# Kernel optimization log

Measured on AMD Instinct MI355X. Metric: run time of the kernel, lower is better.

Reference implementation:

```python
import jax, jax.numpy as jnp
import numpy as np

D_MODEL = 1024
NUM_HEADS = 16
HEAD_DIM = D_MODEL // NUM_HEADS
THETA = 10000.0


def setup_inputs() -> dict:
    key = jax.random.key(0)
    k1, k2, k3 = jax.random.split(key, 3)
    B, S = 4, 2048
    x = jax.random.normal(k1, (B, S, D_MODEL), dtype=jnp.float32)
    token_positions = jnp.arange(S, dtype=jnp.int32)
    std_qkv = 2.0 / (D_MODEL + 3 * D_MODEL)
    std_o = 2.0 / (D_MODEL + D_MODEL)
    W_qkv = jax.random.normal(k2, (3 * D_MODEL, D_MODEL), dtype=jnp.float32) * std_qkv
    W_o = jax.random.normal(k3, (D_MODEL, D_MODEL), dtype=jnp.float32) * std_o
    return {"x": x, "token_positions": token_positions, "W_qkv": W_qkv, "W_o": W_o}


def _apply_rope(x, positions):
    # x: [B, H, S, d]; positions: [S]
    d = x.shape[-1]
    inv_freq = 1.0 / THETA ** (2.0 * jnp.arange(0, d // 2, dtype=jnp.float32) / d)
    angle = positions.astype(jnp.float32)[:, None] * inv_freq[None, :]  # [S, d/2]
    cos, sin = jnp.cos(angle), jnp.sin(angle)
    x1, x2 = x[..., 0::2], x[..., 1::2]
    rot = jnp.stack([x1 * cos - x2 * sin, x2 * cos + x1 * sin], axis=-1)
    return rot.reshape(x.shape)


def reference(x, token_positions, W_qkv, W_o):
    B, S, D = x.shape
    H, hd = NUM_HEADS, HEAD_DIM
    qkv = jnp.einsum('bsi,ji->bsj', x, W_qkv)            # [B, S, 3D]
    qkv = qkv.reshape(B, S, 3, H, hd).transpose(2, 0, 3, 1, 4)  # [3, B, H, S, hd]
    q, k, v = qkv[0], qkv[1], qkv[2]
    q = _apply_rope(q, token_positions)
    k = _apply_rope(k, token_positions)
    scores = jnp.einsum('bhqd,bhkd->bhqk', q, k) / jnp.sqrt(jnp.float32(hd))
    causal = jnp.tril(jnp.ones((S, S), dtype=bool))
    scores = jnp.where(causal, scores, -jnp.inf)
    probs = jax.nn.softmax(scores, axis=-1)
    attn = jnp.einsum('bhqk,bhkd->bhqd', probs, v)       # [B, H, S, hd]
    attn = attn.transpose(0, 2, 1, 3).reshape(B, S, D)
    return jnp.einsum('bsi,ji->bsj', attn, W_o)
```

## Files before the change

kernel.cpp:

```cpp
#include <hip/hip_runtime.h>

#define B_ 4
#define S_ 2048
#define D_ 1024
#define H_ 16
#define HD_ 64
#define M_ (B_*S_)
#define NQKV_ (3*D_)

typedef _Float16 f16;
typedef __attribute__((ext_vector_type(4))) _Float16 f16x4;
typedef __attribute__((ext_vector_type(8))) _Float16 f16x8;
typedef __attribute__((ext_vector_type(4))) float f32x4;

__device__ __forceinline__ void gload_lds16(const void* g, void* lds) {
  __builtin_amdgcn_global_load_lds(
      (const __attribute__((address_space(1))) void*)g,
      (__attribute__((address_space(3))) void*)lds, 16, 0, 0);
}

__global__ void cast_kernel(const float* __restrict__ in, f16* __restrict__ out) {
  size_t i = (size_t)(blockIdx.x * 256 + threadIdx.x) * 8;
  float4 a = *reinterpret_cast<const float4*>(in + i);
  float4 b = *reinterpret_cast<const float4*>(in + i + 4);
  f16x8 o;
  o[0] = (f16)a.x; o[1] = (f16)a.y; o[2] = (f16)a.z; o[3] = (f16)a.w;
  o[4] = (f16)b.x; o[5] = (f16)b.y; o[6] = (f16)b.z; o[7] = (f16)b.w;
  *reinterpret_cast<f16x8*>(out + i) = o;
}

__global__ void trig_kernel(const int* __restrict__ pos, float2* __restrict__ tab) {
  int idx = blockIdx.x * 256 + threadIdx.x;
  int s = idx >> 5, t = idx & 31;
  float p = (float)pos[s];
  float invf = exp2f((float)t * -0.4152410118609203f);
  float sn, cs;
  sincosf(p * invf, &sn, &cs);
  tab[idx] = float2{cs, sn};
}

template <int MODE>
__global__ __launch_bounds__(256)
void gemm_bt(const f16* __restrict__ A, const f16* __restrict__ Bt,
             void* __restrict__ Cout, const float2* __restrict__ tab,
             f16* __restrict__ kout, f16* __restrict__ vtout,
             int M, int N, int K) {
  __shared__ __align__(16) f16 As[128 * 64];
  __shared__ __align__(16) f16 Bs[128 * 64];
  const int tid = threadIdx.x;
  const int w = tid >> 6, l = tid & 63;
  const int nM = M >> 7;
  const int bm = (blockIdx.x % nM) << 7;
  const int bn = (blockIdx.x / nM) << 7;
  const int wr = (w >> 1) << 6;
  const int wc = (w & 1) << 6;
  const int lr = l & 15;
  const int lk = (l >> 4) << 3;
  const int orow = (l >> 4) << 2;
  const int srow = tid >> 3;
  const int sc8 = (tid & 7) * 8;

  f32x4 acc[4][4];
  #pragma unroll
  for (int i = 0; i < 4; ++i)
    #pragma unroll
    for (int j = 0; j < 4; ++j) acc[i][j] = f32x4{0.f, 0.f, 0.f, 0.f};

  for (int k0 = 0; k0 < K; k0 += 64) {
    __syncthreads();
    #pragma unroll
    for (int i = 0; i < 4; ++i) {
      gload_lds16(A + (size_t)(bm + i * 32 + srow) * K + k0 + sc8,
                  (void*)(As + (i * 256 + w * 64) * 8));
      gload_lds16(Bt + (size_t)(bn + i * 32 + srow) * K + k0 + sc8,
                  (void*)(Bs + (i * 256 + w * 64) * 8));
    }
    __syncthreads();
    #pragma unroll
    for (int t = 0; t < 2; ++t) {
      f16x8 af[4], bfr[4];
      #pragma unroll
      for (int mi = 0; mi < 4; ++mi)
        af[mi] = *reinterpret_cast<const f16x8*>(As + (wr + mi * 16 + lr) * 64 + t * 32 + lk);
      #pragma unroll
      for (int ni = 0; ni < 4; ++ni)
        bfr[ni] = *reinterpret_cast<const f16x8*>(Bs + (wc + ni * 16 + lr) * 64 + t * 32 + lk);
      #pragma unroll
      for (int mi = 0; mi < 4; ++mi)
        #pragma unroll
        for (int ni = 0; ni < 4; ++ni)
          acc[mi][ni] = __builtin_amdgcn_mfma_f32_16x16x32_f16(bfr[ni], af[mi], acc[mi][ni], 0, 0, 0);
    }
  }

  if (MODE == 0) {
    const int which = bn >> 10;
    const int h = ((bn + wc) >> 6) & (H_ - 1);
    if (which < 2) {
      f16* dst = which ? kout : (f16*)Cout;
      const float qs = which ? 1.0f : 0.125f * 1.4426950408889634f;
      #pragma unroll
      for (int mi = 0; mi < 4; ++mi) {
        int m = bm + wr + mi * 16 + lr;
        int b = m >> 11, s = m & (S_ - 1);
        size_t rowbase = ((size_t)(b * H_ + h) * S_ + s) * HD_;
        const float4* trow = reinterpret_cast<const float4*>(tab + (size_t)s * 32);
        #pragma unroll
        for (int ni = 0; ni < 4; ++ni) {
          int d0 = ni * 16 + orow;
          float4 cssn = trow[d0 >> 2];
          float x0 = acc[mi][ni][0], x1 = acc[mi][ni][1];
          float x2 = acc[mi][ni][2], x3 = acc[mi][ni][3];
          f16x4 ov;
          ov[0] = (f16)((x0 * cssn.x - x1 * cssn.y) * qs);
          ov[1] = (f16)((x1 * cssn.x + x0 * cssn.y) * qs);
          ov[2] = (f16)((x2 * cssn.z - x3 * cssn.w) * qs);
          ov[3] = (f16)((x3 * cssn.z + x2 * cssn.w) * qs);
          *reinterpret_cast<f16x4*>(&dst[rowbase + d0]) = ov;
        }
      }
    } else {
      #pragma unroll
      for (int mi = 0; mi < 4; ++mi) {
        int m = bm + wr + mi * 16 + lr;
        int b = m >> 11, s = m & (S_ - 1);
        size_t base = (size_t)(b * H_ + h) * (HD_ * S_) + s;
        #pragma unroll
        for (int ni = 0; ni < 4; ++ni)
          #pragma unroll
          for (int r = 0; r < 4; ++r)
            vtout[base + (size_t)(ni * 16 + orow + r) * S_] = (f16)acc[mi][ni][r];
      }
    }
  } else {
    float* C = (float*)Cout;
    #pragma unroll
    for (int mi = 0; mi < 4; ++mi) {
      int m = bm + wr + mi * 16 + lr;
      #pragma unroll
      for (int ni = 0; ni < 4; ++ni) {
        int n = bn + wc + ni * 16 + orow;
        *reinterpret_cast<float4*>(&C[(size_t)m * N + n]) =
            float4{acc[mi][ni][0], acc[mi][ni][1], acc[mi][ni][2], acc[mi][ni][3]};
      }
    }
  }
}

__global__ __launch_bounds__(256)
void attn_kernel(const f16* __restrict__ q, const f16* __restrict__ k,
                 const f16* __restrict__ vt, f16* __restrict__ attn_out) {
  __shared__ __align__(16) f16 Ks[64 * 64];
  __shared__ __align__(16) f16 Vs[64 * 64];
  __shared__ __align__(16) f16 Ps[4][16 * 72];
  const int tid = threadIdx.x, w = tid >> 6, l = tid & 63;
  const int lr = l & 15, lk = (l >> 4) << 3, orow = (l >> 4) << 2;
  const int bh = blockIdx.x & 63;
  const int qt = 31 - (int)(blockIdx.x >> 6);
  const int q0 = qt << 6;
  const size_t bhoff = (size_t)bh * (S_ * HD_);
  const size_t vtoff = (size_t)bh * (HD_ * S_);
  const int srow = tid >> 3;
  const int sc8 = (tid & 7) * 8;
  const int ssw = sc8 ^ ((srow & 7) << 3);
  const int swz = (lr & 7) << 3;
  const int h = bh & (H_ - 1), b = bh >> 4;
  const int qg = q0 + w * 16 + lr;

  f16x8 qf[2];
  #pragma unroll
  for (int t = 0; t < 2; ++t)
    qf[t] = *reinterpret_cast<const f16x8*>(q + bhoff + (size_t)qg * HD_ + t * 32 + lk);

  f32x4 o[4];
  float m_run = -1e30f, l_run = 0.f;
  #pragma unroll
  for (int i = 0; i < 4; ++i) o[i] = f32x4{0.f, 0.f, 0.f, 0.f};

  const int ntiles = qt + 1;
  for (int it = 0; it < ntiles; ++it) {
    const int kv0 = it << 6;
    __syncthreads();
    #pragma unroll
    for (int i = 0; i < 2; ++i) {
      gload_lds16(k + bhoff + (size_t)(kv0 + i * 32 + srow) * HD_ + ssw,
                  (void*)(Ks + (i * 256 + w * 64) * 8));
      gload_lds16(vt + vtoff + (size_t)(i * 32 + srow) * S_ + kv0 + ssw,
                  (void*)(Vs + (i * 256 + w * 64) * 8));
    }
    __syncthreads();

    f32x4 sacc[4];
    #pragma unroll
    for (int ni = 0; ni < 4; ++ni) sacc[ni] = f32x4{0.f, 0.f, 0.f, 0.f};
    #pragma unroll
    for (int t = 0; t < 2; ++t) {
      #pragma unroll
      for (int ni = 0; ni < 4; ++ni) {
        f16x8 kf = *reinterpret_cast<const f16x8*>(Ks + (ni * 16 + lr) * 64 + ((t * 32 + lk) ^ swz));
        sacc[ni] = __builtin_amdgcn_mfma_f32_16x16x32_f16(kf, qf[t], sacc[ni], 0, 0, 0);
      }
    }
    if (it == ntiles - 1) {
      #pragma unroll
      for (int ni = 0; ni < 4; ++ni) {
        #pragma unroll
        for (int r = 0; r < 4; ++r) {
          int kvg = kv0 + ni * 16 + orow + r;
          if (kvg > qg) sacc[ni][r] = -1e30f;
        }
      }
    }

    f32x4 m4 = sacc[0];
    #pragma unroll
    for (int ni = 1; ni < 4; ++ni)
      #pragma unroll
      for (int r = 0; r < 4; ++r) m4[r] = fmaxf(m4[r], sacc[ni][r]);
    float mloc = fmaxf(fmaxf(m4[0], m4[1]), fmaxf(m4[2], m4[3]));
    mloc = fmaxf(mloc, __shfl_xor(mloc, 16));
    mloc = fmaxf(mloc, __shfl_xor(mloc, 32));
    float mn = fmaxf(m_run, mloc);
    float scale = exp2f(m_run - mn);
    m_run = mn;
    #pragma unroll
    for (int ni = 0; ni < 4; ++ni)
      #pragma unroll
      for (int r = 0; r < 4; ++r) sacc[ni][r] = exp2f(sacc[ni][r] - mn);
    f32x4 s4 = sacc[0];
    #pragma unroll
    for (int ni = 1; ni < 4; ++ni)
      #pragma unroll
      for (int r = 0; r < 4; ++r) s4[r] += sacc[ni][r];
    float sloc = (s4[0] + s4[1]) + (s4[2] + s4[3]);
    sloc += __shfl_xor(sloc, 16);
    sloc += __shfl_xor(sloc, 32);
    l_run = l_run * scale + sloc;
    #pragma unroll
    for (int ni = 0; ni < 4; ++ni)
      #pragma unroll
      for (int r = 0; r < 4; ++r) o[ni][r] *= scale;

    #pragma unroll
    for (int ni = 0; ni < 4; ++ni) {
      f16x4 pk;
      #pragma unroll
      for (int r = 0; r < 4; ++r) pk[r] = (f16)sacc[ni][r];
      *reinterpret_cast<f16x4*>(&Ps[w][lr * 72 + ni * 16 + orow]) = pk;
    }

    #pragma unroll
    for (int t = 0; t < 2; ++t) {
      f16x8 pf = *reinterpret_cast<const f16x8*>(&Ps[w][lr * 72 + t * 32 + lk]);
      #pragma unroll
      for (int ni = 0; ni < 4; ++ni) {
        f16x8 vf = *reinterpret_cast<const f16x8*>(Vs + (ni * 16 + lr) * 64 + ((t * 32 + lk) ^ swz));
        o[ni] = __builtin_amdgcn_mfma_f32_16x16x32_f16(vf, pf, o[ni], 0, 0, 0);
      }
    }
  }

  float rl = 1.0f / l_run;
  #pragma unroll
  for (int ni = 0; ni < 4; ++ni) {
    f16x4 ov;
    #pragma unroll
    for (int r = 0; r < 4; ++r) ov[r] = (f16)(o[ni][r] * rl);
    *reinterpret_cast<f16x4*>(
        &attn_out[(size_t)(b * S_ + qg) * D_ + h * HD_ + ni * 16 + orow]) = ov;
  }
}

extern "C" void kernel_launch(void* const* d_in, const int* in_sizes, int n_in,
                              void* d_out, int out_size, void* d_ws, size_t ws_size,
                              hipStream_t stream) {
  const float* x    = (const float*)d_in[0];
  const int*   pos  = (const int*)d_in[1];
  const float* wqkv = (const float*)d_in[2];
  const float* wo   = (const float*)d_in[3];
  float* out = (float*)d_out;

  const size_t BHSD = (size_t)B_ * H_ * S_ * HD_;
  f16* xb    = (f16*)d_ws;
  f16* wqkvb = xb + (size_t)M_ * D_;
  f16* wob   = wqkvb + (size_t)NQKV_ * D_;
  f16* qb    = wob + (size_t)D_ * D_;
  f16* kb    = qb + BHSD;
  f16* vtb   = kb + BHSD;
  f16* attnb = vtb + BHSD;
  float2* tab = (float2*)(attnb + BHSD);

  cast_kernel<<<(M_ * D_) / 2048, 256, 0, stream>>>(x, xb);
  cast_kernel<<<(NQKV_ * D_) / 2048, 256, 0, stream>>>(wqkv, wqkvb);
  cast_kernel<<<(D_ * D_) / 2048, 256, 0, stream>>>(wo, wob);
  trig_kernel<<<(S_ * 32) / 256, 256, 0, stream>>>(pos, tab);

  gemm_bt<0><<<(M_ / 128) * (NQKV_ / 128), 256, 0, stream>>>(
      xb, wqkvb, (void*)qb, tab, kb, vtb, M_, NQKV_, D_);

  attn_kernel<<<64 * 32, 256, 0, stream>>>(qb, kb, vtb, attnb);

  gemm_bt<1><<<(M_ / 128) * (D_ / 128), 256, 0, stream>>>(
      attnb, wob, (void*)out, nullptr, nullptr, nullptr, M_, D_, D_);
}
```

Before: 216.2 us.

## Use 32x32x16 MFMA with 128-row query tiles in attention kernel

Switches the flash-attention kernel from 16x16x32 MFMAs with 64-query tiles to 32x32x16 MFMAs with 128-query tiles, so each wave handles 32 query rows. Each K/V tile loaded into LDS is now reused by twice as many queries, halving K/V traffic per query. Waves whose rows lie entirely before the current KV tile skip the compute. The P buffer gets an XOR swizzle, and the launch-bounds hint asks for 4 blocks per CU. The risks are higher register pressure from 16-wide accumulators, half as many blocks to spread over the GPU, and idle waves on the diagonal tiles.

```diff
diff --git a/kernel.cpp b/kernel.cpp
--- a/kernel.cpp
+++ b/kernel.cpp
@@ -12,6 +12,7 @@
 typedef __attribute__((ext_vector_type(4))) _Float16 f16x4;
 typedef __attribute__((ext_vector_type(8))) _Float16 f16x8;
 typedef __attribute__((ext_vector_type(4))) float f32x4;
+typedef __attribute__((ext_vector_type(16))) float f32x16;
 
 __device__ __forceinline__ void gload_lds16(const void* g, void* lds) {
   __builtin_amdgcn_global_load_lds(
@@ -147,128 +148,138 @@
   }
 }
 
-__global__ __launch_bounds__(256)
+__global__ __launch_bounds__(256, 4)
 void attn_kernel(const f16* __restrict__ q, const f16* __restrict__ k,
                  const f16* __restrict__ vt, f16* __restrict__ attn_out) {
   __shared__ __align__(16) f16 Ks[64 * 64];
   __shared__ __align__(16) f16 Vs[64 * 64];
-  __shared__ __align__(16) f16 Ps[4][16 * 72];
-  const int tid = threadIdx.x, w = tid >> 6, l = tid & 63;
-  const int lr = l & 15, lk = (l >> 4) << 3, orow = (l >> 4) << 2;
+  __shared__ __align__(16) f16 Ps[4][32 * 64];
+  const int tid = threadIdx.x, wq = tid >> 6, l = tid & 63;
+  const int lq = l & 31, hi = l >> 5;
   const int bh = blockIdx.x & 63;
-  const int qt = 31 - (int)(blockIdx.x >> 6);
-  const int q0 = qt << 6;
+  const int qt = 15 - (int)(blockIdx.x >> 6);
+  const int q0 = qt << 7;
   const size_t bhoff = (size_t)bh * (S_ * HD_);
   const size_t vtoff = (size_t)bh * (HD_ * S_);
   const int srow = tid >> 3;
   const int sc8 = (tid & 7) * 8;
   const int ssw = sc8 ^ ((srow & 7) << 3);
-  const int swz = (lr & 7) << 3;
+  const int swz = (lq & 7) << 3;
   const int h = bh & (H_ - 1), b = bh >> 4;
-  const int qg = q0 + w * 16 + lr;
-
-  f16x8 qf[2];
+  const int wqmin = q0 + wq * 32;
+  const int qrow = wqmin + lq;
+
+  f16x8 qf[4];
   #pragma unroll
-  for (int t = 0; t < 2; ++t)
-    qf[t] = *reinterpret_cast<const f16x8*>(q + bhoff + (size_t)qg * HD_ + t * 32 + lk);
-
-  f32x4 o[4];
+  for (int s = 0; s < 4; ++s)
+    qf[s] = *reinterpret_cast<const f16x8*>(q + bhoff + (size_t)qrow * HD_ + s * 16 + hi * 8);
+
+  f32x16 o[2];
   float m_run = -1e30f, l_run = 0.f;
   #pragma unroll
-  for (int i = 0; i < 4; ++i) o[i] = f32x4{0.f, 0.f, 0.f, 0.f};
-
-  const int ntiles = qt + 1;
+  for (int i = 0; i < 2; ++i)
+    #pragma unroll
+    for (int r = 0; r < 16; ++r) o[i][r] = 0.f;
+
+  f16* Pw = &Ps[wq][0];
+  const int ntiles = 2 * qt + 2;
   for (int it = 0; it < ntiles; ++it) {
     const int kv0 = it << 6;
     __syncthreads();
     #pragma unroll
     for (int i = 0; i < 2; ++i) {
       gload_lds16(k + bhoff + (size_t)(kv0 + i * 32 + srow) * HD_ + ssw,
-                  (void*)(Ks + (i * 256 + w * 64) * 8));
+                  (void*)(Ks + (i * 256 + wq * 64) * 8));
       gload_lds16(vt + vtoff + (size_t)(i * 32 + srow) * S_ + kv0 + ssw,
-                  (void*)(Vs + (i * 256 + w * 64) * 8));
+                  (void*)(Vs + (i * 256 + wq * 64) * 8));
     }
     __syncthreads();
 
-    f32x4 sacc[4];
-    #pragma unroll
-    for (int ni = 0; ni < 4; ++ni) sacc[ni] = f32x4{0.f, 0.f, 0.f, 0.f};
-    #pragma unroll
-    for (int t = 0; t < 2; ++t) {
-      #pragma unroll
-      for (int ni = 0; ni < 4; ++ni) {
-        f16x8 kf = *reinterpret_cast<const f16x8*>(Ks + (ni * 16 + lr) * 64 + ((t * 32 + lk) ^ swz));
-        sacc[ni] = __builtin_amdgcn_mfma_f32_16x16x32_f16(kf, qf[t], sacc[ni], 0, 0, 0);
-      }
-    }
-    if (it == ntiles - 1) {
-      #pragma unroll
-      for (int ni = 0; ni < 4; ++ni) {
-        #pragma unroll
-        for (int r = 0; r < 4; ++r) {
-          int kvg = kv0 + ni * 16 + orow + r;
-          if (kvg > qg) sacc[ni][r] = -1e30f;
-        }
-      }
-    }
-
-    f32x4 m4 = sacc[0];
-    #pragma unroll
-    for (int ni = 1; ni < 4; ++ni)
-      #pragma unroll
-      for (int r = 0; r < 4; ++r) m4[r] = fmaxf(m4[r], sacc[ni][r]);
-    float mloc = fmaxf(fmaxf(m4[0], m4[1]), fmaxf(m4[2], m4[3]));
-    mloc = fmaxf(mloc, __shfl_xor(mloc, 16));
-    mloc = fmaxf(mloc, __shfl_xor(mloc, 32));
-    float mn = fmaxf(m_run, mloc);
-    float scale = exp2f(m_run - mn);
-    m_run = mn;
-    #pragma unroll
-    for (int ni = 0; ni < 4; ++ni)
-      #pragma unroll
-      for (int r = 0; r < 4; ++r) sacc[ni][r] = exp2f(sacc[ni][r] - mn);
-    f32x4 s4 = sacc[0];
-    #pragma unroll
-    for (int ni = 1; ni < 4; ++ni)
-      #pragma unroll
-      for (int r = 0; r < 4; ++r) s4[r] += sacc[ni][r];
-    float sloc = (s4[0] + s4[1]) + (s4[2] + s4[3]);
-    sloc += __shfl_xor(sloc, 16);
-    sloc += __shfl_xor(sloc, 32);
-    l_run = l_run * scale + sloc;
-    #pragma unroll
-    for (int ni = 0; ni < 4; ++ni)
-      #pragma unroll
-      for (int r = 0; r < 4; ++r) o[ni][r] *= scale;
-
-    #pragma unroll
-    for (int ni = 0; ni < 4; ++ni) {
-      f16x4 pk;
-      #pragma unroll
-      for (int r = 0; r < 4; ++r) pk[r] = (f16)sacc[ni][r];
-      *reinterpret_cast<f16x4*>(&Ps[w][lr * 72 + ni * 16 + orow]) = pk;
-    }
-
-    #pragma unroll
-    for (int t = 0; t < 2; ++t) {
-      f16x8 pf = *reinterpret_cast<const f16x8*>(&Ps[w][lr * 72 + t * 32 + lk]);
-      #pragma unroll
-      for (int ni = 0; ni < 4; ++ni) {
-        f16x8 vf = *reinterpret_cast<const f16x8*>(Vs + (ni * 16 + lr) * 64 + ((t * 32 + lk) ^ swz));
-        o[ni] = __builtin_amdgcn_mfma_f32_16x16x32_f16(vf, pf, o[ni], 0, 0, 0);
-      }
+    if (kv0 <= wqmin + 31) {
+      f32x16 sacc[2];
+      #pragma unroll
+      for (int kh = 0; kh < 2; ++kh) {
+        #pragma unroll
+        for (int r = 0; r < 16; ++r) sacc[kh][r] = 0.f;
+        #pragma unroll
+        for (int s = 0; s < 4; ++s) {
+          f16x8 kf = *reinterpret_cast<const f16x8*>(
+              Ks + (kh * 32 + lq) * 64 + ((s * 16 + hi * 8) ^ swz));
+          sacc[kh] = __builtin_amdgcn_mfma_f32_32x32x16_f16(kf, qf[s], sacc[kh], 0, 0, 0);
+        }
+      }
+      if (kv0 + 63 >= wqmin) {
+        #pragma unroll
+        for (int kh = 0; kh < 2; ++kh)
+          #pragma unroll
+          for (int r = 0; r < 16; ++r) {
+            int kvg = kv0 + kh * 32 + (r & 3) + 8 * (r >> 2) + 4 * hi;
+            if (kvg > qrow) sacc[kh][r] = -1e30f;
+          }
+      }
+
+      float mloc = -1e30f;
+      #pragma unroll
+      for (int kh = 0; kh < 2; ++kh)
+        #pragma unroll
+        for (int r = 0; r < 16; ++r) mloc = fmaxf(mloc, sacc[kh][r]);
+      mloc = fmaxf(mloc, __shfl_xor(mloc, 32));
+      float mn = fmaxf(m_run, mloc);
+      float scale = exp2f(m_run - mn);
+      m_run = mn;
+      float sloc = 0.f;
+      #pragma unroll
+      for (int kh = 0; kh < 2; ++kh)
+        #pragma unroll
+        for (int r = 0; r < 16; ++r) {
+          sacc[kh][r] = exp2f(sacc[kh][r] - mn);
+          sloc += sacc[kh][r];
+        }
+      sloc += __shfl_xor(sloc, 32);
+      l_run = l_run * scale + sloc;
+      #pragma unroll
+      for (int i = 0; i < 2; ++i)
+        #pragma unroll
+        for (int r = 0; r < 16; ++r) o[i][r] *= scale;
+
+      #pragma unroll
+      for (int kh = 0; kh < 2; ++kh)
+        #pragma unroll
+        for (int qd = 0; qd < 4; ++qd) {
+          f16x4 pk;
+          #pragma unroll
+          for (int r = 0; r < 4; ++r) pk[r] = (f16)sacc[kh][qd * 4 + r];
+          int kvb = kh * 32 + qd * 8 + hi * 4;
+          *reinterpret_cast<f16x4*>(&Pw[lq * 64 + (kvb ^ swz)]) = pk;
+        }
+
+      f16x8 pf[4];
+      #pragma unroll
+      for (int s2 = 0; s2 < 4; ++s2)
+        pf[s2] = *reinterpret_cast<const f16x8*>(&Pw[lq * 64 + ((s2 * 16 + hi * 8) ^ swz)]);
+      #pragma unroll
+      for (int dh = 0; dh < 2; ++dh)
+        #pragma unroll
+        for (int s2 = 0; s2 < 4; ++s2) {
+          f16x8 vf = *reinterpret_cast<const f16x8*>(
+              Vs + (dh * 32 + lq) * 64 + ((s2 * 16 + hi * 8) ^ swz));
+          o[dh] = __builtin_amdgcn_mfma_f32_32x32x16_f16(vf, pf[s2], o[dh], 0, 0, 0);
+        }
     }
   }
 
   float rl = 1.0f / l_run;
   #pragma unroll
-  for (int ni = 0; ni < 4; ++ni) {
-    f16x4 ov;
-    #pragma unroll
-    for (int r = 0; r < 4; ++r) ov[r] = (f16)(o[ni][r] * rl);
-    *reinterpret_cast<f16x4*>(
-        &attn_out[(size_t)(b * S_ + qg) * D_ + h * HD_ + ni * 16 + orow]) = ov;
-  }
+  for (int dh = 0; dh < 2; ++dh)
+    #pragma unroll
+    for (int qd = 0; qd < 4; ++qd) {
+      f16x4 ov;
+      #pragma unroll
+      for (int r = 0; r < 4; ++r) ov[r] = (f16)(o[dh][qd * 4 + r] * rl);
+      int d0 = dh * 32 + qd * 8 + hi * 4;
+      *reinterpret_cast<f16x4*>(
+          &attn_out[(size_t)(b * S_ + qrow) * D_ + h * HD_ + d0]) = ov;
+    }
 }
 
 extern "C" void kernel_launch(void* const* d_in, const int* in_sizes, int n_in,
@@ -298,7 +309,7 @@
   gemm_bt<0><<<(M_ / 128) * (NQKV_ / 128), 256, 0, stream>>>(
       xb, wqkvb, (void*)qb, tab, kb, vtb, M_, NQKV_, D_);
 
-  attn_kernel<<<64 * 32, 256, 0, stream>>>(qb, kb, vtb, attnb);
+  attn_kernel<<<64 * 16, 256, 0, stream>>>(qb, kb, vtb, attnb);
 
   gemm_bt<1><<<(M_ / 128) * (D_ / 128), 256, 0, stream>>>(
       attnb, wob, (void*)out, nullptr, nullptr, nullptr, M_, D_, D_);
```

New measurement: 207.0 us. -4.2%, faster.
